# Performance work log

Hardware: AMD Instinct MI355X
Metric: run time of the kernel (lower is better)

## Reference

```python
import jax, jax.numpy as jnp
import numpy as np

B, C, N = 64, 81, 8732


def setup_inputs() -> dict:
    key = jax.random.key(0)
    k1, k2, k3, k4, k5 = jax.random.split(key, 5)
    ploc = jax.random.normal(k1, (B, 4, N), dtype=jnp.float32)
    plabel = jax.random.normal(k2, (B, C, N), dtype=jnp.float32)
    # gloc: uniform, shifted positive so gwh/dwh log is well-defined
    gloc = jax.random.uniform(k3, (B, 4, N), dtype=jnp.float32) * 0.9 + 0.05
    glabel = jax.random.randint(k4, (B, N), 0, C, dtype=jnp.int64)
    # default boxes: keep widths/heights bounded away from 0
    dboxes = jax.random.uniform(k5, (1, 4, N), dtype=jnp.float32) * 0.9 + 0.1
    return {"ploc": ploc, "plabel": plabel, "gloc": gloc, "glabel": glabel, "dboxes": dboxes}


def _smooth_l1(x):
    ax = jnp.abs(x)
    return jnp.where(ax < 1.0, 0.5 * ax * ax, ax - 0.5)


def reference(ploc, plabel, gloc, glabel, dboxes):
    mask = glabel > 0                       # [B, N] positive anchors
    num_pos = mask.sum(axis=1)              # [B]

    # encode ground-truth boxes as offsets relative to default boxes
    dxy, dwh = dboxes[:, :2, :], dboxes[:, 2:, :]
    gxy = (gloc[:, :2, :] - dxy) / dwh
    gwh = jnp.log(gloc[:, 2:, :] / dwh)
    goff = jnp.concatenate([gxy, gwh], axis=1)  # [B, 4, N]

    # localization loss: smooth L1 summed over coords, masked to positives
    loc = _smooth_l1(ploc - goff).sum(axis=1)   # [B, N]
    loc_loss = (mask * loc).sum(axis=1)         # [B]

    # per-anchor cross entropy
    logp = jax.nn.log_softmax(plabel, axis=1)   # [B, C, N]
    closs = -jnp.take_along_axis(logp, glabel[:, None, :], axis=1)[:, 0, :]  # [B, N]

    # hard negative mining via rank (double argsort, descending)
    con_neg = jnp.where(mask, 0.0, closs)
    con_idx = jnp.argsort(-con_neg, axis=1)
    con_rank = jnp.argsort(con_idx, axis=1)
    neg_num = jnp.minimum(3 * num_pos, N)[:, None]
    neg_mask = con_rank < neg_num
    con_loss = (closs * (mask.astype(jnp.float32) + neg_mask.astype(jnp.float32))).sum(axis=1)

    total = loc_loss + con_loss
    num_mask = (num_pos > 0).astype(jnp.float32)
    npos = jnp.clip(num_pos.astype(jnp.float32), 1e-6)
    return ((total * num_mask) / npos).mean()
```

## Files before the change

### kernel.cpp

```cpp
#include <hip/hip_runtime.h>
#include <math.h>

#define BATCH 64
#define NCLS  81
#define NANCH 8732
#define NG    (NANCH / 4)
#define BLK   256
#define BPB   ((NG + BLK - 1) / BLK)

__device__ inline float smooth_l1(float d) {
    float a = fabsf(d);
    return (a < 1.f) ? 0.5f * a * a : a - 0.5f;
}


__global__ __launch_bounds__(256) void k_main(
    const float* __restrict__ ploc, const float* __restrict__ plabel,
    const float* __restrict__ gloc, const int* __restrict__ glabel,
    const float* __restrict__ dboxes, float4* __restrict__ ws)
{
    const int b   = blockIdx.x / BPB;
    const int gid = (blockIdx.x % BPB) * BLK + threadIdx.x;

    float l_loc = 0.f, l_posc = 0.f, l_negc = 0.f;
    int   l_cnt = 0;

    if (gid < NG) {
        const int4 gi = ((const int4*)(glabel + (size_t)b * NANCH))[gid];
        const int g[4] = {gi.x, gi.y, gi.z, gi.w};

        const float4* pploc = (const float4*)(ploc + (size_t)b * 4 * NANCH);
        const float4* pgloc = (const float4*)(gloc + (size_t)b * 4 * NANCH);
        const float4* pdb   = (const float4*)dboxes;
        float4 Pv[4], Gv[4], Dv[4];
#pragma unroll
        for (int ch = 0; ch < 4; ++ch) {
            Pv[ch] = pploc[ch * NG + gid];
            Gv[ch] = pgloc[ch * NG + gid];
            Dv[ch] = pdb[ch * NG + gid];
        }

        const float4* pl4 = (const float4*)(plabel + (size_t)b * NCLS * NANCH) + gid;
        float s[4]  = {0.f, 0.f, 0.f, 0.f};
        float xg[4] = {0.f, 0.f, 0.f, 0.f};
#pragma unroll 9
        for (int c = 0; c < NCLS; ++c) {
            const float4 xv = pl4[(size_t)c * NG];
            const float x[4] = {xv.x, xv.y, xv.z, xv.w};
#pragma unroll
            for (int i = 0; i < 4; ++i) {
                s[i] += __expf(x[i]);
                xg[i] = (c == g[i]) ? x[i] : xg[i];
            }
        }

        const float P[4][4] = {{Pv[0].x,Pv[0].y,Pv[0].z,Pv[0].w},
                               {Pv[1].x,Pv[1].y,Pv[1].z,Pv[1].w},
                               {Pv[2].x,Pv[2].y,Pv[2].z,Pv[2].w},
                               {Pv[3].x,Pv[3].y,Pv[3].z,Pv[3].w}};
        const float G[4][4] = {{Gv[0].x,Gv[0].y,Gv[0].z,Gv[0].w},
                               {Gv[1].x,Gv[1].y,Gv[1].z,Gv[1].w},
                               {Gv[2].x,Gv[2].y,Gv[2].z,Gv[2].w},
                               {Gv[3].x,Gv[3].y,Gv[3].z,Gv[3].w}};
        const float D[4][4] = {{Dv[0].x,Dv[0].y,Dv[0].z,Dv[0].w},
                               {Dv[1].x,Dv[1].y,Dv[1].z,Dv[1].w},
                               {Dv[2].x,Dv[2].y,Dv[2].z,Dv[2].w},
                               {Dv[3].x,Dv[3].y,Dv[3].z,Dv[3].w}};

#pragma unroll
        for (int i = 0; i < 4; ++i) {
            float closs = __logf(s[i]) - xg[i];
            float gx = (G[0][i] - D[0][i]) / D[2][i];
            float gy = (G[1][i] - D[1][i]) / D[3][i];
            float gw = __logf(G[2][i] / D[2][i]);
            float gh = __logf(G[3][i] / D[3][i]);
            float loc_i = smooth_l1(P[0][i] - gx) + smooth_l1(P[1][i] - gy)
                        + smooth_l1(P[2][i] - gw) + smooth_l1(P[3][i] - gh);
            bool  mk = g[i] > 0;
            l_loc  += mk ? loc_i : 0.f;
            l_posc += mk ? closs : 0.f;
            l_negc += mk ? 0.f : closs;
            l_cnt  += mk ? 1 : 0;
        }
    }

#pragma unroll
    for (int off = 32; off; off >>= 1) {
        l_loc  += __shfl_down(l_loc, off);
        l_posc += __shfl_down(l_posc, off);
        l_negc += __shfl_down(l_negc, off);
        l_cnt  += __shfl_down(l_cnt, off);
    }
    __shared__ float sl[4], sp[4], sn[4];
    __shared__ int   sc[4];
    const int wave = threadIdx.x >> 6, lane = threadIdx.x & 63;
    if (lane == 0) { sl[wave] = l_loc; sp[wave] = l_posc; sn[wave] = l_negc; sc[wave] = l_cnt; }
    __syncthreads();
    if (threadIdx.x == 0) {
        float a = 0.f, p = 0.f, n = 0.f; int ct = 0;
#pragma unroll
        for (int w = 0; w < 4; ++w) { a += sl[w]; p += sp[w]; n += sn[w]; ct += sc[w]; }
        ws[blockIdx.x] = make_float4(a, p, n, (float)ct);
    }
}

__device__ float closs_at(const float* __restrict__ plabel, int b, int n, int g) {
    const float* p = plabel + (size_t)b * NCLS * NANCH + n;
    float m = -INFINITY, s = 0.f, xg = 0.f;
    for (int c = 0; c < NCLS; ++c) {
        float x = p[(size_t)c * NANCH];
        float nm = fmaxf(m, x);
        float e  = __expf(fminf(m, x) - nm);
        s = (x > m) ? s * e + 1.f : s + e;
        m = nm;
        if (c == g) xg = x;
    }
    return m + __logf(s) - xg;
}

__global__ __launch_bounds__(256) void k_fin(
    const float* __restrict__ plabel, const int* __restrict__ glabel,
    const float4* __restrict__ ws, float* __restrict__ out)
{
    const float4* partials = ws;
    const int tid = threadIdx.x;
    __shared__ float s_contrib[BATCH];
    __shared__ float s_loc[BATCH], s_posc[BATCH], s_negc[BATCH];
    __shared__ int   s_np[BATCH], s_cold[BATCH];
    __shared__ unsigned int hist[256];
    __shared__ unsigned int s_bucket;
    __shared__ long long s_rnext;
    __shared__ float rs[4], rc[4];

    if (tid < BATCH) {
        const int b = tid;
        float loc = 0.f, pc = 0.f, nc = 0.f, cf = 0.f;
#pragma unroll
        for (int j = 0; j < BPB; ++j) {
            float4 v = partials[b * BPB + j];
            loc += v.x; pc += v.y; nc += v.z; cf += v.w;
        }
        const int np = (int)(cf + 0.5f);
        s_loc[b] = loc; s_posc[b] = pc; s_negc[b] = nc; s_np[b] = np;
        s_contrib[b] = 0.f;
        s_cold[b] = 0;
        if (np > 0) {
            long long K = 3LL * np; if (K > NANCH) K = NANCH;
            const int nn = NANCH - np;
            if ((long long)nn <= K) {
                long long extra = K - nn;
                if (extra >= np) {
                    float total = loc + 2.f * pc + nc;
                    s_contrib[b] = total / fmaxf((float)np, 1e-6f) * (1.f / BATCH);
                } else {
                    s_cold[b] = 1;
                }
            } else {
                s_cold[b] = 2;
            }
        }
    }
    __syncthreads();

    for (int b = 0; b < BATCH; ++b) {
        const int mode = s_cold[b];
        if (mode == 0) continue;
        const int np = s_np[b];
        long long K = 3LL * np; if (K > NANCH) K = NANCH;
        const int nn = NANCH - np;

        if (mode == 1) {
            long long extra = K - nn;
            if (tid < 64) {
                long long cnt = 0; float sum = 0.f;
                for (int base = 0; base < NANCH; base += 64) {
                    int n = base + tid;
                    int gl = (n < NANCH) ? glabel[(size_t)b * NANCH + n] : 0;
                    bool p = gl > 0;
                    unsigned long long bal = __ballot(p);
                    int r = __popcll(bal & ((1ull << tid) - 1ull));
                    if (p && (cnt + r) < extra) sum += closs_at(plabel, b, n, gl);
                    cnt += (long long)__popcll(bal);
                }
#pragma unroll
                for (int off = 32; off; off >>= 1) sum += __shfl_down(sum, off);
                if (tid == 0) {
                    float total = s_loc[b] + s_posc[b] + (s_negc[b] + sum);
                    s_contrib[b] = total / fmaxf((float)np, 1e-6f) * (1.f / BATCH);
                }
            }
        } else {
            unsigned int prefix = 0;
            long long r = K;
            for (int level = 3; level >= 0; --level) {
                const int shift = level * 8;
                hist[tid] = 0u;
                __syncthreads();
                const unsigned int pmask =
                    (level == 3) ? 0u : (0xFFFFFFFFu << ((level + 1) * 8));
                for (int n = tid; n < NANCH; n += 256) {
                    int gl = glabel[(size_t)b * NANCH + n];
                    float v = (gl > 0) ? 0.f : fmaxf(closs_at(plabel, b, n, gl), 0.f);
                    unsigned int bits = __float_as_uint(v);
                    if ((bits & pmask) == (prefix & pmask))
                        atomicAdd(&hist[(bits >> shift) & 255u], 1u);
                }
                __syncthreads();
                if (tid == 0) {
                    long long acc_c = 0; int bsel = 0;
                    for (int i = 255; i >= 0; --i) {
                        if (acc_c + (long long)hist[i] >= r) { bsel = i; break; }
                        acc_c += hist[i];
                    }
                    s_bucket = (unsigned int)bsel;
                    s_rnext  = r - acc_c;
                }
                __syncthreads();
                prefix |= (s_bucket << shift);
                r = s_rnext;
                __syncthreads();
            }
            const float T = __uint_as_float(prefix);
            float lsum = 0.f, lcnt = 0.f;
            for (int n = tid; n < NANCH; n += 256) {
                int gl = glabel[(size_t)b * NANCH + n];
                float v = (gl > 0) ? 0.f : fmaxf(closs_at(plabel, b, n, gl), 0.f);
                if (v > T) { lsum += v; lcnt += 1.f; }
            }
#pragma unroll
            for (int off = 32; off; off >>= 1) {
                lsum += __shfl_down(lsum, off);
                lcnt += __shfl_down(lcnt, off);
            }
            const int wave = tid >> 6, lane = tid & 63;
            if (lane == 0) { rs[wave] = lsum; rc[wave] = lcnt; }
            __syncthreads();
            if (tid == 0) {
                float gsum = 0.f, gcnt = 0.f;
#pragma unroll
                for (int w = 0; w < 4; ++w) { gsum += rs[w]; gcnt += rc[w]; }
                float sel = gsum + ((float)K - gcnt) * T;
                float total = s_loc[b] + s_posc[b] + sel;
                s_contrib[b] = total / fmaxf((float)np, 1e-6f) * (1.f / BATCH);
            }
        }
        __syncthreads();
    }
    __syncthreads();

    if (tid == 0) {
        float acc = 0.f;
#pragma unroll
        for (int b = 0; b < BATCH; ++b) acc += s_contrib[b];
        out[0] = acc;
    }
}

extern "C" void kernel_launch(void* const* d_in, const int* in_sizes, int n_in,
                              void* d_out, int out_size, void* d_ws, size_t ws_size,
                              hipStream_t stream) {
    const float* ploc   = (const float*)d_in[0];
    const float* plabel = (const float*)d_in[1];
    const float* gloc   = (const float*)d_in[2];
    const int*   glabel = (const int*)d_in[3];
    const float* dboxes = (const float*)d_in[4];
    float* out = (float*)d_out;
    float4* ws = (float4*)d_ws;

    hipLaunchKernelGGL(k_main, dim3(BATCH * BPB), dim3(256), 0, stream,
                       ploc, plabel, gloc, glabel, dboxes, ws);
    hipLaunchKernelGGL(k_fin, dim3(1), dim3(256), 0, stream,
                       plabel, glabel, ws, out);
}
```

Baseline: 280.7 us.

## Double-buffer class-logit loads with nontemporal prefetch in main loss kernel

```diff
diff --git a/kernel.cpp b/kernel.cpp
--- a/kernel.cpp
+++ b/kernel.cpp
@@ -7,6 +7,10 @@
 #define NG    (NANCH / 4)
 #define BLK   256
 #define BPB   ((NG + BLK - 1) / BLK)
+#define NBLK  (BATCH * BPB)
+
+typedef float __attribute__((ext_vector_type(4))) f4;
+typedef int   __attribute__((ext_vector_type(4))) i4;
 
 __device__ inline float smooth_l1(float d) {
     float a = fabsf(d);
@@ -14,7 +18,7 @@
 }
 
 
-__global__ __launch_bounds__(256) void k_main(
+__global__ __launch_bounds__(256, 2) void k_main(
     const float* __restrict__ ploc, const float* __restrict__ plabel,
     const float* __restrict__ gloc, const int* __restrict__ glabel,
     const float* __restrict__ dboxes, float4* __restrict__ ws)
@@ -26,56 +30,68 @@
     int   l_cnt = 0;
 
     if (gid < NG) {
-        const int4 gi = ((const int4*)(glabel + (size_t)b * NANCH))[gid];
+        const i4 gi = __builtin_nontemporal_load(
+            (const i4*)(glabel + (size_t)b * NANCH) + gid);
         const int g[4] = {gi.x, gi.y, gi.z, gi.w};
 
-        const float4* pploc = (const float4*)(ploc + (size_t)b * 4 * NANCH);
-        const float4* pgloc = (const float4*)(gloc + (size_t)b * 4 * NANCH);
-        const float4* pdb   = (const float4*)dboxes;
-        float4 Pv[4], Gv[4], Dv[4];
-#pragma unroll
-        for (int ch = 0; ch < 4; ++ch) {
-            Pv[ch] = pploc[ch * NG + gid];
-            Gv[ch] = pgloc[ch * NG + gid];
-            Dv[ch] = pdb[ch * NG + gid];
-        }
-
-        const float4* pl4 = (const float4*)(plabel + (size_t)b * NCLS * NANCH) + gid;
+        const f4* pl4 = (const f4*)(plabel + (size_t)b * NCLS * NANCH) + gid;
+
         float s[4]  = {0.f, 0.f, 0.f, 0.f};
         float xg[4] = {0.f, 0.f, 0.f, 0.f};
-#pragma unroll 9
-        for (int c = 0; c < NCLS; ++c) {
-            const float4 xv = pl4[(size_t)c * NG];
-            const float x[4] = {xv.x, xv.y, xv.z, xv.w};
-#pragma unroll
-            for (int i = 0; i < 4; ++i) {
-                s[i] += __expf(x[i]);
-                xg[i] = (c == g[i]) ? x[i] : xg[i];
-            }
-        }
-
-        const float P[4][4] = {{Pv[0].x,Pv[0].y,Pv[0].z,Pv[0].w},
-                               {Pv[1].x,Pv[1].y,Pv[1].z,Pv[1].w},
-                               {Pv[2].x,Pv[2].y,Pv[2].z,Pv[2].w},
-                               {Pv[3].x,Pv[3].y,Pv[3].z,Pv[3].w}};
-        const float G[4][4] = {{Gv[0].x,Gv[0].y,Gv[0].z,Gv[0].w},
-                               {Gv[1].x,Gv[1].y,Gv[1].z,Gv[1].w},
-                               {Gv[2].x,Gv[2].y,Gv[2].z,Gv[2].w},
-                               {Gv[3].x,Gv[3].y,Gv[3].z,Gv[3].w}};
-        const float D[4][4] = {{Dv[0].x,Dv[0].y,Dv[0].z,Dv[0].w},
-                               {Dv[1].x,Dv[1].y,Dv[1].z,Dv[1].w},
-                               {Dv[2].x,Dv[2].y,Dv[2].z,Dv[2].w},
-                               {Dv[3].x,Dv[3].y,Dv[3].z,Dv[3].w}};
+
+        f4 A[9], B[9];
+#define PF(BUF, BASE)                                                       \
+        do { _Pragma("unroll")                                              \
+            for (int j = 0; j < 9; ++j)                                     \
+                BUF[j] = __builtin_nontemporal_load(                        \
+                    pl4 + (size_t)((BASE) + j) * NG);                       \
+        } while (0)
+#define CS(BUF, BASE)                                                       \
+        do { _Pragma("unroll")                                              \
+            for (int j = 0; j < 9; ++j) {                                   \
+                const f4 xv = BUF[j];                                       \
+                _Pragma("unroll")                                           \
+                for (int i = 0; i < 4; ++i) {                               \
+                    const float x = xv[i];                                  \
+                    s[i] += __expf(x);                                      \
+                    xg[i] = (((BASE) + j) == g[i]) ? x : xg[i];             \
+                }                                                           \
+            }                                                               \
+        } while (0)
+
+        PF(A, 0);
+        PF(B, 9);   CS(A, 0);
+        PF(A, 18);  CS(B, 9);
+        PF(B, 27);  CS(A, 18);
+        PF(A, 36);  CS(B, 27);
+        PF(B, 45);  CS(A, 36);
+        PF(A, 54);  CS(B, 45);
+        PF(B, 63);  CS(A, 54);
+        PF(A, 72);  CS(B, 63);
+        CS(A, 72);
+#undef PF
+#undef CS
+
+        const f4* pploc = (const f4*)(ploc + (size_t)b * 4 * NANCH);
+        const f4* pgloc = (const f4*)(gloc + (size_t)b * 4 * NANCH);
+        const f4* pdb   = (const f4*)dboxes;
+        f4 Pv[4], Gv[4], Dv[4];
+#pragma unroll
+        for (int ch = 0; ch < 4; ++ch) {
+            Pv[ch] = __builtin_nontemporal_load(pploc + ch * NG + gid);
+            Gv[ch] = __builtin_nontemporal_load(pgloc + ch * NG + gid);
+            Dv[ch] = __builtin_nontemporal_load(pdb   + ch * NG + gid);
+        }
 
 #pragma unroll
         for (int i = 0; i < 4; ++i) {
             float closs = __logf(s[i]) - xg[i];
-            float gx = (G[0][i] - D[0][i]) / D[2][i];
-            float gy = (G[1][i] - D[1][i]) / D[3][i];
-            float gw = __logf(G[2][i] / D[2][i]);
-            float gh = __logf(G[3][i] / D[3][i]);
-            float loc_i = smooth_l1(P[0][i] - gx) + smooth_l1(P[1][i] - gy)
-                        + smooth_l1(P[2][i] - gw) + smooth_l1(P[3][i] - gh);
+            float gx = (Gv[0][i] - Dv[0][i]) / Dv[2][i];
+            float gy = (Gv[1][i] - Dv[1][i]) / Dv[3][i];
+            float gw = __logf(Gv[2][i] / Dv[2][i]);
+            float gh = __logf(Gv[3][i] / Dv[3][i]);
+            float loc_i = smooth_l1(Pv[0][i] - gx) + smooth_l1(Pv[1][i] - gy)
+                        + smooth_l1(Pv[2][i] - gw) + smooth_l1(Pv[3][i] - gh);
             bool  mk = g[i] > 0;
             l_loc  += mk ? loc_i : 0.f;
             l_posc += mk ? closs : 0.f;
@@ -267,7 +283,7 @@
     float* out = (float*)d_out;
     float4* ws = (float4*)d_ws;
 
-    hipLaunchKernelGGL(k_main, dim3(BATCH * BPB), dim3(256), 0, stream,
+    hipLaunchKernelGGL(k_main, dim3(NBLK), dim3(256), 0, stream,
                        ploc, plabel, gloc, glabel, dboxes, ws);
     hipLaunchKernelGGL(k_fin, dim3(1), dim3(256), 0, stream,
                        plabel, glabel, ws, out);
```

Result: faster. 260.3 us (-7.3%).
